# Kernel optimization log

Hardware: AMD Instinct MI355X
Metric: run time of the kernel (lower is better)

The kernel has to match this reference:

```python
import jax, jax.numpy as jnp
import numpy as np

B, L, N, M = 2, 4, 2048, 1024
K, DIV = 32, 4
S = K // DIV  # maxpool window along neighbor axis
F1 = 128      # prev features
PF = 64       # lift output point-feature dim
OUT = 256
EPS = 1e-5


def setup_inputs() -> dict:
    key = jax.random.key(0)
    ks = jax.random.split(key, 12)
    C_in = PF + F1  # 192, conv input channels
    return {
        "points": jax.random.normal(ks[0], (B, L, N, 3), jnp.float32),
        "queries": jax.random.normal(ks[1], (B, L, M, 3), jnp.float32),
        "feat_prev": jax.random.normal(ks[2], (B, L, N, F1), jnp.float32),
        # Lift params
        "bn1_g": jnp.ones((3,), jnp.float32),
        "bn1_b": jnp.zeros((3,), jnp.float32),
        "w1": jax.random.normal(ks[3], (PF // 2, 3), jnp.float32) * 0.3,
        "b1": jnp.zeros((PF // 2,), jnp.float32),
        "bn2_g": jnp.ones((PF // 2,), jnp.float32),
        "bn2_b": jnp.zeros((PF // 2,), jnp.float32),
        "w2": jax.random.normal(ks[4], (PF, PF // 2), jnp.float32) * 0.1,
        "b2": jnp.zeros((PF,), jnp.float32),
        # conv = BatchNorm3d(C_in) + Conv3d(C_in, OUT, (1,1,DIV))
        "bnc_g": jnp.ones((C_in,), jnp.float32),
        "bnc_b": jnp.zeros((C_in,), jnp.float32),
        "conv_w": jax.random.normal(ks[5], (OUT, C_in, DIV), jnp.float32) * 0.05,
        "conv_b": jnp.zeros((OUT,), jnp.float32),
    }


def _bn(x, g, b):
    """Training-mode batchnorm, channel = last axis (equivalent to the
    torch transpose(1,4)->BatchNorm3d->transpose(1,4) pattern)."""
    ax = tuple(range(x.ndim - 1))
    m = x.mean(ax)
    v = x.var(ax)  # biased variance, as torch uses for normalization
    return (x - m) * jax.lax.rsqrt(v + EPS) * g + b


_gather = jax.vmap(jax.vmap(lambda arr, idx: arr[idx]))  # over B, L


def reference(points, queries, feat_prev,
              bn1_g, bn1_b, w1, b1, bn2_g, bn2_b, w2, b2,
              bnc_g, bnc_b, conv_w, conv_b):
    # ---- KNN (cdist + topk, fully batched) ----
    pn = jnp.sum(points * points, -1)          # (B,L,N)
    qn = jnp.sum(queries * queries, -1)        # (B,L,M)
    cross = jnp.einsum('blmc,blnc->blmn', queries, points)
    d2 = qn[..., None] + pn[:, :, None, :] - 2.0 * cross  # (B,L,M,N)
    idx = jax.lax.top_k(-d2, K)[1]             # (B,L,M,K) ascending distance

    nn_pts = _gather(points, idx)              # (B,L,M,K,3)
    local = queries[:, :, :, None, :] - nn_pts # center - neighbors

    # ---- Lift MLP (with batchnorm) ----
    h = _bn(local, bn1_g, bn1_b)
    h = jax.nn.relu(jnp.einsum('blmki,oi->blmko', h, w1) + b1)
    h = _bn(h, bn2_g, bn2_b)
    h = jax.nn.relu(jnp.einsum('blmki,oi->blmko', h, w2) + b2)  # (B,L,M,K,PF)

    # ---- gather prev features, concat ----
    fp = _gather(feat_prev, idx)               # (B,L,M,K,F1)
    feat = jnp.concatenate([h, fp], axis=-1)   # (B,L,M,K,C_in)

    # ---- maxpool over neighbor shells: window S, stride S along K ----
    C = feat.shape[-1]
    fm = feat.reshape(B, L, M, DIV, S, C).max(axis=4)  # (B,L,M,DIV,C)

    # ---- BatchNorm3d(C_in) + Conv3d(C_in, OUT, (1,1,DIV)) ----
    fm = _bn(fm, bnc_g, bnc_b)
    out = jnp.einsum('blmdc,ocd->blmo', fm, conv_w) + conv_b  # (B,L,M,OUT)
    return out
```

## Files before the change

### kernel.cpp

```cpp
#include <hip/hip_runtime.h>
#include <cstdint>

#define B_    2
#define L_    4
#define N_    2048
#define M_    1024
#define K_    32
#define DIV_  4
#define S_    8
#define F1_   128
#define PF_   64
#define CIN_  192
#define OUT_  256
#define EPS_  1e-5f

#define BL_   (B_*L_)
#define BLM_  (BL_*M_)
#define NPTS_ (BLM_*K_)
#define ROWS_ (BLM_*DIV_)

#define OFF_FMH  0
#define OFF_IDX  3145728
#define OFF_LOC  3407872
#define OFF_W1F  4456448
#define OFF_B1F  4456544
#define OFF_W2F  4456576
#define OFF_B2F  4458624
#define OFF_WCB  4458688
#define OFF_BCF  4556992
#define OFF_P2   4557248
#define OFF_P3   4573632

typedef __attribute__((ext_vector_type(8))) short short8;
typedef __attribute__((ext_vector_type(4))) short short4v;
typedef __attribute__((ext_vector_type(4))) float f32x4;

__device__ __forceinline__ unsigned short f2bf(float f)
{
    unsigned u = __float_as_uint(f);
    unsigned r = (u + 0x7FFFu + ((u >> 16) & 1u)) >> 16;
    return (unsigned short)r;
}
__device__ __forceinline__ float bf2f(unsigned short h)
{
    unsigned u = ((unsigned)h) << 16;
    return __uint_as_float(u);
}

__global__ __launch_bounds__(512) void k_knn(const float* __restrict__ points,
                                             const float* __restrict__ queries,
                                             int*   __restrict__ idxbuf,
                                             float* __restrict__ local4,
                                             float* __restrict__ p1)
{
#pragma clang fp contract(off)
    __shared__ float4 pt[N_];
    __shared__ unsigned bufN[8][64];
    __shared__ float  wred[8][8];

    const int t    = threadIdx.x;
    const int lane = t & 63;
    const int wv   = t >> 6;
    const int bl   = blockIdx.x >> 7;
    const int m    = ((blockIdx.x & 127) << 3) + wv;

    const float* P = points  + (size_t)bl * (N_*3);
    const float* Q = queries + (size_t)bl * (M_*3);

    for (int n = t; n < N_; n += 512) {
        float x = P[n*3], y = P[n*3+1], z = P[n*3+2];
        float pn = (x*x + y*y) + z*z;
        pt[n] = make_float4(x, y, z, pn);
    }
    __syncthreads();

    const float qx = Q[m*3], qy = Q[m*3+1], qz = Q[m*3+2];
    const float qn = (qx*qx + qy*qy) + qz*qz;
    const double qxd = (double)qx, qyd = (double)qy, qzd = (double)qz;

    auto uAkey = [&](unsigned n) -> unsigned {
        const float4 p4 = pt[n & 2047];
        float cross = (qx*p4.x + qy*p4.y) + qz*p4.z;
        float d2f = (qn + p4.w) - 2.0f*cross;
        unsigned uA = __float_as_uint(d2f);
        return (uA & 0x80000000u) ? ~uA : (uA | 0x80000000u);
    };
    auto uBkey = [&](unsigned n) -> unsigned long long {
        const float4 p4 = pt[n & 2047];
        double dx = qxd - (double)p4.x, dy = qyd - (double)p4.y, dz = qzd - (double)p4.z;
        double d2d = dx*dx + dy*dy + dz*dz;
        unsigned long long uB = (unsigned long long)__double_as_longlong(d2d);
        uB = (uB & 0x8000000000000000ULL) ? ~uB : (uB | 0x8000000000000000ULL);
        return (uB & ~2047ULL) | (unsigned long long)(n & 2047);
    };
    auto cmp_less = [&](unsigned pa, unsigned pn, unsigned ca, unsigned cn) -> bool {
        bool eq = (pa == ca);
        bool pl = eq ? (pn < cn) : (pa < ca);
        bool realtie = eq && (ca != 0xFFFFFFFFu);
        if (realtie) pl = (uBkey(pn) < uBkey(cn));
        return pl;
    };

    unsigned Aa = 0xFFFFFFFFu;
    unsigned An = 2048u + lane;
    unsigned thrA = 0xFFFFFFFFu;
    int bufcnt = 0;

    auto flushfn = [&]() {
        unsigned sa, sn;
        if (lane < bufcnt) { sn = bufN[wv][lane]; sa = uAkey(sn); }
        else               { sa = 0xFFFFFFFFu;    sn = 2048u + lane; }
        for (int k = 2; k <= 64; k <<= 1) {
            for (int j = k >> 1; j >= 1; j >>= 1) {
                unsigned pa = __shfl_xor(sa, j);
                unsigned pn = __shfl_xor(sn, j);
                bool wantMin = (((lane & k) == 0) == ((lane & j) == 0));
                bool pl = cmp_less(pa, pn, sa, sn);
                if (pl == wantMin) { sa = pa; sn = pn; }
            }
        }
        int src = (31 - lane) & 63;
        unsigned ba = __shfl(sa, src);
        unsigned bn = __shfl(sn, src);
        if (lane < 32) {
            if (cmp_less(ba, bn, Aa, An)) { Aa = ba; An = bn; }
        }
        for (int j = 16; j >= 1; j >>= 1) {
            unsigned pa = __shfl_xor(Aa, j);
            unsigned pn = __shfl_xor(An, j);
            bool wantMin = ((lane & j) == 0);
            bool pl = cmp_less(pa, pn, Aa, An);
            if (pl == wantMin) { Aa = pa; An = pn; }
        }
        bufcnt = 0;
        thrA = __shfl(Aa, 31);
    };

    float4 p4 = pt[lane];
    for (int r = 0; r < 32; ++r) {
        const int n = r*64 + lane;
        float4 p4n = p4;
        if (r < 31) p4n = pt[n + 64];
        float cross = (qx*p4.x + qy*p4.y) + qz*p4.z;
        float d2f = (qn + p4.w) - 2.0f*cross;
        unsigned uA = __float_as_uint(d2f);
        uA = (uA & 0x80000000u) ? ~uA : (uA | 0x80000000u);
        p4 = p4n;

        bool lt = (uA <= thrA);
        unsigned long long mask = __ballot(lt);
        int cnt = __builtin_popcountll(mask);
        if (cnt == 0) continue;
        if (bufcnt + cnt > 64) {
            flushfn();
            lt = (uA <= thrA);
            mask = __ballot(lt);
            cnt = __builtin_popcountll(mask);
            if (cnt == 0) continue;
        }
        int pos = bufcnt + __builtin_popcountll(mask & ((1ULL << lane) - 1ULL));
        if (lt) bufN[wv][pos] = (unsigned)n;
        bufcnt += cnt;
    }
    if (bufcnt > 0) flushfn();

    const long long base = ((long long)bl * M_ + m) * K_;
    float lx = 0.f, ly = 0.f, lz = 0.f;
    if (lane < 32) {
        const int n = (int)An;
        idxbuf[base + lane] = n;
        const float4 pp = pt[n];
        lx = qx - pp.x; ly = qy - pp.y; lz = qz - pp.z;
        *(float4*)(local4 + (base + lane)*4) = make_float4(lx, ly, lz, 0.f);
    }
    float s0 = lx, s1 = ly, s2 = lz, s3 = lx*lx, s4 = ly*ly, s5 = lz*lz;
#pragma unroll
    for (int off = 32; off; off >>= 1) {
        s0 += __shfl_xor(s0, off); s1 += __shfl_xor(s1, off); s2 += __shfl_xor(s2, off);
        s3 += __shfl_xor(s3, off); s4 += __shfl_xor(s4, off); s5 += __shfl_xor(s5, off);
    }
    if (lane == 0) {
        wred[wv][0]=s0; wred[wv][1]=s1; wred[wv][2]=s2;
        wred[wv][3]=s3; wred[wv][4]=s4; wred[wv][5]=s5;
    }
    __syncthreads();
    if (t < 6) {
        float s = 0.f;
#pragma unroll
        for (int w = 0; w < 8; ++w) s += wred[w][t];
        p1[(long long)blockIdx.x*8 + t] = s;
    }
}

__global__ __launch_bounds__(256) void k_fold1(const float* __restrict__ p1,
                        const float* __restrict__ w1, const float* __restrict__ b1,
                        const float* __restrict__ g,  const float* __restrict__ bb,
                        float* __restrict__ w1f, float* __restrict__ b1f)
{
    __shared__ float red[6][33];
    __shared__ float s1[3], t1[3];
    const int t = threadIdx.x;
    const int c = t >> 5, i = t & 31;
    if (c < 6) {
        float s = 0.f;
        for (int w = i; w < 1024; w += 32) s += p1[w*8 + c];
        red[c][i] = s;
    }
    __syncthreads();
    if (t < 3) {
        float S = 0.f, Q = 0.f;
        for (int k = 0; k < 32; ++k) { S += red[t][k]; Q += red[t+3][k]; }
        float mean = S / (float)NPTS_;
        float var  = Q / (float)NPTS_ - mean*mean;
        float r = 1.0f / sqrtf(var + EPS_);
        float sc = r * g[t];
        s1[t] = sc; t1[t] = bb[t] - mean*sc;
    }
    __syncthreads();
    if (t < 32) {
        float acc = b1[t];
        for (int i2 = 0; i2 < 3; ++i2) {
            float w = w1[t*3+i2];
            w1f[t*3+i2] = w * s1[i2];
            acc += w * t1[i2];
        }
        b1f[t] = acc;
    }
}

__global__ __launch_bounds__(256) void k_stats2(const float* __restrict__ local4,
                                                const float* __restrict__ w1f,
                                                const float* __restrict__ b1f,
                                                float* __restrict__ p2)
{
    __shared__ float4 pts[1024];
    __shared__ float  sred[4][64];
    const int t = threadIdx.x;
    const int lane = t & 63;
    const int wv   = t >> 6;
    const int base = blockIdx.x * 1024;

    for (int j = t; j < 1024; j += 256)
        pts[j] = *(const float4*)(local4 + (size_t)(base + j) * 4);

    const int ch = lane & 31;
    const float w0 = w1f[ch*3], w1v = w1f[ch*3+1], w2v = w1f[ch*3+2];
    const float bv = b1f[ch];
    __syncthreads();

    float s = 0.f, q = 0.f;
    const int pbase = wv*256 + (lane >> 5);
    for (int it = 0; it < 128; ++it) {
        float4 v = pts[pbase + it*2];
        float h = fmaxf(bv + w0*v.x + w1v*v.y + w2v*v.z, 0.f);
        s += h; q += h*h;
    }
    s += __shfl_xor(s, 32); q += __shfl_xor(q, 32);
    if (lane < 32) { sred[wv][lane] = s; sred[wv][32+lane] = q; }
    __syncthreads();
    if (t < 64)
        p2[blockIdx.x*64 + t] = sred[0][t]+sred[1][t]+sred[2][t]+sred[3][t];
}

__global__ void k_fold2(const float* __restrict__ p2,
                        const float* __restrict__ w2, const float* __restrict__ b2,
                        const float* __restrict__ g,  const float* __restrict__ bb,
                        float* __restrict__ w2f, float* __restrict__ b2f)
{
    __shared__ float s2[32], t2[32];
    int t = threadIdx.x;
    if (t < 32) {
        float S = 0, Q = 0;
        for (int b = 0; b < 256; ++b) { S += p2[b*64+t]; Q += p2[b*64+32+t]; }
        float mean = S / (float)NPTS_;
        float var  = Q / (float)NPTS_ - mean*mean;
        float r = 1.0f / sqrtf(var + EPS_);
        float sc = r * g[t];
        s2[t] = sc; t2[t] = bb[t] - mean*sc;
    }
    __syncthreads();
    float acc = b2[t];
    for (int i = 0; i < 32; ++i) {
        float w = w2[t*32+i];
        w2f[t*32+i] = w * s2[i];
        acc += w * t2[i];
    }
    b2f[t] = acc;
}

__global__ __launch_bounds__(256) void k_shell(const float* __restrict__ feat_prev,
                                               const int*   __restrict__ idxbuf,
                                               const float* __restrict__ local4,
                                               const float* __restrict__ w1f,
                                               const float* __restrict__ b1f,
                                               const float* __restrict__ w2f,
                                               const float* __restrict__ b2f,
                                               unsigned short* __restrict__ fmh)
{
    __shared__ float w1s[96], b1s[32], b2s[64];
    __shared__ float w2s[64][33];
    __shared__ int   idxs[K_];
    __shared__ float locs[K_][4];
    __shared__ __align__(16) float h1s[K_][36];
    __shared__ float fmrow[DIV_][CIN_];

    const int t = threadIdx.x;
    const int lane = t & 63;
    const int wv   = t >> 6;

    for (int j = t; j < 2048; j += 256) { int o = j >> 5, i = j & 31; w2s[o][i] = w2f[j]; }
    if (t < 96) w1s[t] = w1f[t];
    if (t >= 96 && t < 128) b1s[t-96] = b1f[t-96];
    if (t >= 128 && t < 192) b2s[t-128] = b2f[t-128];
    __syncthreads();

    float w2c[32];
#pragma unroll
    for (int i = 0; i < 32; ++i) w2c[i] = w2s[lane][i];
    const float b2v = b2s[lane];

    for (int q = 0; q < 8; ++q) {
        const int blm = (blockIdx.x << 3) + q;
        const long long base = (long long)blm * K_;
        if (t < 32)  idxs[t] = idxbuf[base + t];
        if (t >= 64 && t < 192) ((float*)locs)[t-64] = local4[base*4 + (t-64)];
        __syncthreads();

        for (int j = t; j < 1024; j += 256) {
            int k = j >> 5, o = j & 31;
            float v = b1s[o] + w1s[o*3]*locs[k][0] + w1s[o*3+1]*locs[k][1] + w1s[o*3+2]*locs[k][2];
            h1s[k][o] = fmaxf(v, 0.f);
        }
        __syncthreads();

        {
            float mx = 0.0f;
#pragma unroll
            for (int kk = 0; kk < 8; ++kk) {
                const int k = wv*8 + kk;
                const float4* hp = (const float4*)&h1s[k][0];
                float acc = b2v;
#pragma unroll
                for (int c = 0; c < 8; ++c) {
                    float4 h4 = hp[c];
                    acc += h4.x*w2c[c*4+0];
                    acc += h4.y*w2c[c*4+1];
                    acc += h4.z*w2c[c*4+2];
                    acc += h4.w*w2c[c*4+3];
                }
                mx = fmaxf(mx, fmaxf(acc, 0.f));
            }
            fmrow[wv][lane] = mx;
        }
        {
            const float* fp0 = feat_prev + (size_t)(blm / M_) * N_ * F1_;
#pragma unroll
            for (int ph = 0; ph < 2; ++ph) {
                int d = ph*2 + (t >> 7), c = t & 127;
                float mx = -3.4e38f;
#pragma unroll
                for (int j = 0; j < 8; ++j) {
                    int n = idxs[d*8+j];
                    mx = fmaxf(mx, fp0[(size_t)n*F1_ + c]);
                }
                fmrow[d][64 + c] = mx;
            }
        }
        __syncthreads();
        for (int j = t; j < DIV_*CIN_; j += 256)
            fmh[(size_t)blm*(DIV_*CIN_) + j] = f2bf((&fmrow[0][0])[j]);
        __syncthreads();
    }
}

__global__ void k_stats3(const unsigned short* __restrict__ fmh, float* __restrict__ p3)
{
    const int t = threadIdx.x;
    const int blk = blockIdx.x;
    float s = 0.f, q = 0.f;
    const size_t base = (size_t)blk * 128 * CIN_;
    for (int r = 0; r < 128; ++r) {
        float v = bf2f(fmh[base + (size_t)r*CIN_ + t]);
        s += v; q += v*v;
    }
    p3[blk*384 + t] = s;
    p3[blk*384 + 192 + t] = q;
}

__global__ __launch_bounds__(256) void k_fold3(const float* __restrict__ p3,
                                               const float* __restrict__ conv_w,
                                               const float* __restrict__ conv_b,
                                               const float* __restrict__ g,
                                               const float* __restrict__ bb,
                                               unsigned short* __restrict__ wcfb,
                                               float* __restrict__ bcf)
{
    __shared__ float sc[CIN_], tc[CIN_];
    const int t = threadIdx.x;
    if (t < CIN_) {
        float S = 0, Q = 0;
        for (int b = 0; b < 256; ++b) { S += p3[b*384+t]; Q += p3[b*384+192+t]; }
        float mean = S / (float)ROWS_;
        float var  = Q / (float)ROWS_ - mean*mean;
        float r = 1.0f / sqrtf(var + EPS_);
        float s = r * g[t];
        sc[t] = s; tc[t] = bb[t] - mean*s;
    }
    __syncthreads();
    const int lo = blockIdx.x * 3072;
    for (int j = lo + t; j < lo + 3072; j += 256) {
        int o = j / 768, k = j - o*768;
        int d = k / CIN_, c = k - d*CIN_;
        wcfb[j] = f2bf(conv_w[o*768 + c*4 + d] * sc[c]);
    }
    if (blockIdx.x == 0) {
        float acc = conv_b[t];
        for (int c = 0; c < CIN_; ++c) {
            float tcv = tc[c];
#pragma unroll
            for (int d = 0; d < 4; ++d) acc += tcv * conv_w[t*768 + c*4 + d];
        }
        bcf[t] = acc;
    }
}

__global__ __launch_bounds__(256) void k_gemm(const unsigned short* __restrict__ A,
                                              const unsigned short* __restrict__ Wb,
                                              const float* __restrict__ bias,
                                              float* __restrict__ C)
{
    __shared__ __align__(16) unsigned short As[128][72];
    __shared__ __align__(16) unsigned short Bs[64][72];
    const int t = threadIdx.x;
    const int lane = t & 63;
    const int wv = t >> 6;
    const int row0 = (blockIdx.x >> 2) * 128;
    const int col0 = (blockIdx.x & 3) * 64;
    const int wr = wv >> 1, wc = wv & 1;
    const int r16 = lane & 15, kq = lane >> 4;

    f32x4 acc[4][2];
#pragma unroll
    for (int i = 0; i < 4; ++i)
#pragma unroll
        for (int j = 0; j < 2; ++j) acc[i][j] = (f32x4){0.f,0.f,0.f,0.f};

    for (int kt = 0; kt < 12; ++kt) {
#pragma unroll
        for (int p = 0; p < 4; ++p) {
            int j = p*256 + t;
            int r = j >> 3, kc = (j & 7) * 8;
            *(short8*)&As[r][kc] = *(const short8*)(A + (size_t)(row0 + r)*768 + kt*64 + kc);
        }
#pragma unroll
        for (int p = 0; p < 2; ++p) {
            int j = p*256 + t;
            int r = j >> 3, kc = (j & 7) * 8;
            *(short8*)&Bs[r][kc] = *(const short8*)(Wb + (size_t)(col0 + r)*768 + kt*64 + kc);
        }
        __syncthreads();
#pragma unroll
        for (int ks = 0; ks < 2; ++ks) {
            short8 bf[2];
#pragma unroll
            for (int n = 0; n < 2; ++n) {
                const unsigned short* pb = &Bs[wc*32 + n*16 + r16][ks*32 + kq*4];
                short4v b0 = *(const short4v*)pb;
                short4v b1 = *(const short4v*)(pb + 16);
                bf[n][0]=b0[0]; bf[n][1]=b0[1]; bf[n][2]=b0[2]; bf[n][3]=b0[3];
                bf[n][4]=b1[0]; bf[n][5]=b1[1]; bf[n][6]=b1[2]; bf[n][7]=b1[3];
            }
#pragma unroll
            for (int mf = 0; mf < 4; ++mf) {
                const unsigned short* pa = &As[wr*64 + mf*16 + r16][ks*32 + kq*4];
                short4v a0 = *(const short4v*)pa;
                short4v a1 = *(const short4v*)(pa + 16);
                short8 af;
                af[0]=a0[0]; af[1]=a0[1]; af[2]=a0[2]; af[3]=a0[3];
                af[4]=a1[0]; af[5]=a1[1]; af[6]=a1[2]; af[7]=a1[3];
                acc[mf][0] = __builtin_amdgcn_mfma_f32_16x16x32_bf16(af, bf[0], acc[mf][0], 0, 0, 0);
                acc[mf][1] = __builtin_amdgcn_mfma_f32_16x16x32_bf16(af, bf[1], acc[mf][1], 0, 0, 0);
            }
        }
        __syncthreads();
    }

#pragma unroll
    for (int mf = 0; mf < 4; ++mf) {
#pragma unroll
        for (int n = 0; n < 2; ++n) {
            const int col = col0 + wc*32 + n*16 + r16;
            const float bv = bias[col];
#pragma unroll
            for (int i = 0; i < 4; ++i) {
                int row = row0 + wr*64 + mf*16 + kq*4 + i;
                C[(size_t)row*256 + col] = acc[mf][n][i] + bv;
            }
        }
    }
}

extern "C" void kernel_launch(void* const* d_in, const int* in_sizes, int n_in,
                              void* d_out, int out_size, void* d_ws, size_t ws_size,
                              hipStream_t stream)
{
    const float* points    = (const float*)d_in[0];
    const float* queries   = (const float*)d_in[1];
    const float* feat_prev = (const float*)d_in[2];
    const float* bn1g = (const float*)d_in[3];
    const float* bn1b = (const float*)d_in[4];
    const float* w1   = (const float*)d_in[5];
    const float* b1   = (const float*)d_in[6];
    const float* bn2g = (const float*)d_in[7];
    const float* bn2b = (const float*)d_in[8];
    const float* w2   = (const float*)d_in[9];
    const float* b2   = (const float*)d_in[10];
    const float* bncg = (const float*)d_in[11];
    const float* bncb = (const float*)d_in[12];
    const float* convw= (const float*)d_in[13];
    const float* convb= (const float*)d_in[14];

    float* ws   = (float*)d_ws;
    unsigned short* fmh = (unsigned short*)(ws + OFF_FMH);
    int*   idxb = (int*)(ws + OFF_IDX);
    float* loc4 = ws + OFF_LOC;
    float* w1f  = ws + OFF_W1F;
    float* b1f  = ws + OFF_B1F;
    float* w2f  = ws + OFF_W2F;
    float* b2f  = ws + OFF_B2F;
    unsigned short* wcfb = (unsigned short*)(ws + OFF_WCB);
    float* bcf  = ws + OFF_BCF;
    float* p1   = ws + OFF_FMH;
    float* p2   = ws + OFF_P2;
    float* p3   = ws + OFF_P3;

    k_knn   <<<1024, 512, 0, stream>>>(points, queries, idxb, loc4, p1);
    k_fold1 <<<1, 256, 0, stream>>>(p1, w1, b1, bn1g, bn1b, w1f, b1f);
    k_stats2<<<256, 256, 0, stream>>>(loc4, w1f, b1f, p2);
    k_fold2 <<<1, 64, 0, stream>>>(p2, w2, b2, bn2g, bn2b, w2f, b2f);
    k_shell <<<BLM_/8, 256, 0, stream>>>(feat_prev, idxb, loc4, w1f, b1f, w2f, b2f, fmh);
    k_stats3<<<256, 192, 0, stream>>>(fmh, p3);
    k_fold3 <<<64, 256, 0, stream>>>(p3, convw, convb, bncg, bncb, wcfb, bcf);
    k_gemm  <<<256, 256, 0, stream>>>(fmh, wcfb, bcf, (float*)d_out);
}
```

Baseline: 173.6 us.

## Fuse BN1 fold into stats2 and BN3 statistics into shell kernel

Merges the single-block k_fold1 into k_stats2, so every block redundantly reduces the p1 partials and folds BN1 itself, with block 0 writing w1f/b1f. It also computes the per-channel sum and sum-of-squares of the bf16 pooled features inside k_shell as they are written, removing the separate k_stats3 pass that re-read fmh. This drops two launches and one full read of the pooled tensor. In exchange, k_fold3 must now reduce 1024 partial rows instead of 256 with a single thread per channel, and k_stats2 adds a redundant p1 reduction in every block.

Measured after the change: 206.2 us. 1.19x slower.

```diff
diff --git a/kernel.cpp b/kernel.cpp
--- a/kernel.cpp
+++ b/kernel.cpp
@@ -192,20 +192,35 @@
     }
 }
 
-__global__ __launch_bounds__(256) void k_fold1(const float* __restrict__ p1,
-                        const float* __restrict__ w1, const float* __restrict__ b1,
-                        const float* __restrict__ g,  const float* __restrict__ bb,
-                        float* __restrict__ w1f, float* __restrict__ b1f)
+__global__ __launch_bounds__(256) void k_stats2(const float* __restrict__ local4,
+                                                const float* __restrict__ p1,
+                                                const float* __restrict__ w1,
+                                                const float* __restrict__ b1,
+                                                const float* __restrict__ g1,
+                                                const float* __restrict__ bb1,
+                                                float* __restrict__ w1f,
+                                                float* __restrict__ b1f,
+                                                float* __restrict__ p2)
 {
     __shared__ float red[6][33];
-    __shared__ float s1[3], t1[3];
+    __shared__ float s1v[3], t1v[3];
+    __shared__ float4 pts[1024];
+    __shared__ float  sred[4][64];
     const int t = threadIdx.x;
-    const int c = t >> 5, i = t & 31;
-    if (c < 6) {
-        float s = 0.f;
-        for (int w = i; w < 1024; w += 32) s += p1[w*8 + c];
-        red[c][i] = s;
-    }
+    const int lane = t & 63;
+    const int wv   = t >> 6;
+    const int base = blockIdx.x * 1024;
+
+    {
+        const int c = t >> 5, i = t & 31;
+        if (c < 6) {
+            float s = 0.f;
+            for (int w = i; w < 1024; w += 32) s += p1[w*8 + c];
+            red[c][i] = s;
+        }
+    }
+    for (int j = t; j < 1024; j += 256)
+        pts[j] = *(const float4*)(local4 + (size_t)(base + j) * 4);
     __syncthreads();
     if (t < 3) {
         float S = 0.f, Q = 0.f;
@@ -213,40 +228,25 @@
         float mean = S / (float)NPTS_;
         float var  = Q / (float)NPTS_ - mean*mean;
         float r = 1.0f / sqrtf(var + EPS_);
-        float sc = r * g[t];
-        s1[t] = sc; t1[t] = bb[t] - mean*sc;
-    }
-    __syncthreads();
-    if (t < 32) {
+        float sc = r * g1[t];
+        s1v[t] = sc; t1v[t] = bb1[t] - mean*sc;
+    }
+    __syncthreads();
+    if (blockIdx.x == 0 && t < 32) {
         float acc = b1[t];
-        for (int i2 = 0; i2 < 3; ++i2) {
-            float w = w1[t*3+i2];
-            w1f[t*3+i2] = w * s1[i2];
-            acc += w * t1[i2];
+        for (int i = 0; i < 3; ++i) {
+            float w = w1[t*3+i];
+            w1f[t*3+i] = w * s1v[i];
+            acc += w * t1v[i];
         }
         b1f[t] = acc;
     }
-}
-
-__global__ __launch_bounds__(256) void k_stats2(const float* __restrict__ local4,
-                                                const float* __restrict__ w1f,
-                                                const float* __restrict__ b1f,
-                                                float* __restrict__ p2)
-{
-    __shared__ float4 pts[1024];
-    __shared__ float  sred[4][64];
-    const int t = threadIdx.x;
-    const int lane = t & 63;
-    const int wv   = t >> 6;
-    const int base = blockIdx.x * 1024;
-
-    for (int j = t; j < 1024; j += 256)
-        pts[j] = *(const float4*)(local4 + (size_t)(base + j) * 4);
 
     const int ch = lane & 31;
-    const float w0 = w1f[ch*3], w1v = w1f[ch*3+1], w2v = w1f[ch*3+2];
-    const float bv = b1f[ch];
-    __syncthreads();
+    const float wa = w1[ch*3], wb = w1[ch*3+1], wc = w1[ch*3+2];
+    const float w0 = wa*s1v[0], w1v = wb*s1v[1], w2v = wc*s1v[2];
+    float bv = b1[ch];
+    bv += wa*t1v[0]; bv += wb*t1v[1]; bv += wc*t1v[2];
 
     float s = 0.f, q = 0.f;
     const int pbase = wv*256 + (lane >> 5);
@@ -295,7 +295,8 @@
                                                const float* __restrict__ b1f,
                                                const float* __restrict__ w2f,
                                                const float* __restrict__ b2f,
-                                               unsigned short* __restrict__ fmh)
+                                               unsigned short* __restrict__ fmh,
+                                               float* __restrict__ p3)
 {
     __shared__ float w1s[96], b1s[32], b2s[64];
     __shared__ float w2s[64][33];
@@ -303,6 +304,7 @@
     __shared__ float locs[K_][4];
     __shared__ __align__(16) float h1s[K_][36];
     __shared__ float fmrow[DIV_][CIN_];
+    __shared__ float ps[768], pq[768];
 
     const int t = threadIdx.x;
     const int lane = t & 63;
@@ -318,6 +320,9 @@
 #pragma unroll
     for (int i = 0; i < 32; ++i) w2c[i] = w2s[lane][i];
     const float b2v = b2s[lane];
+
+    float sacc0 = 0.f, sacc1 = 0.f, sacc2 = 0.f;
+    float qacc0 = 0.f, qacc1 = 0.f, qacc2 = 0.f;
 
     for (int q = 0; q < 8; ++q) {
         const int blm = (blockIdx.x << 3) + q;
@@ -367,24 +372,31 @@
             }
         }
         __syncthreads();
-        for (int j = t; j < DIV_*CIN_; j += 256)
-            fmh[(size_t)blm*(DIV_*CIN_) + j] = f2bf((&fmrow[0][0])[j]);
+        {
+            const size_t ob = (size_t)blm*(DIV_*CIN_);
+            unsigned short h0 = f2bf((&fmrow[0][0])[t]);
+            unsigned short h1 = f2bf((&fmrow[0][0])[t+256]);
+            unsigned short h2 = f2bf((&fmrow[0][0])[t+512]);
+            fmh[ob + t]       = h0;
+            fmh[ob + t + 256] = h1;
+            fmh[ob + t + 512] = h2;
+            float v0 = bf2f(h0), v1 = bf2f(h1), v2 = bf2f(h2);
+            sacc0 += v0; qacc0 += v0*v0;
+            sacc1 += v1; qacc1 += v1*v1;
+            sacc2 += v2; qacc2 += v2*v2;
+        }
         __syncthreads();
     }
-}
-
-__global__ void k_stats3(const unsigned short* __restrict__ fmh, float* __restrict__ p3)
-{
-    const int t = threadIdx.x;
-    const int blk = blockIdx.x;
-    float s = 0.f, q = 0.f;
-    const size_t base = (size_t)blk * 128 * CIN_;
-    for (int r = 0; r < 128; ++r) {
-        float v = bf2f(fmh[base + (size_t)r*CIN_ + t]);
-        s += v; q += v*v;
-    }
-    p3[blk*384 + t] = s;
-    p3[blk*384 + 192 + t] = q;
+
+    ps[t] = sacc0; ps[t+256] = sacc1; ps[t+512] = sacc2;
+    pq[t] = qacc0; pq[t+256] = qacc1; pq[t+512] = qacc2;
+    __syncthreads();
+    if (t < CIN_) {
+        float s = ps[t] + ps[t+192] + ps[t+384] + ps[t+576];
+        float q = pq[t] + pq[t+192] + pq[t+384] + pq[t+576];
+        p3[(size_t)blockIdx.x*384 + t] = s;
+        p3[(size_t)blockIdx.x*384 + 192 + t] = q;
+    }
 }
 
 __global__ __launch_bounds__(256) void k_fold3(const float* __restrict__ p3,
@@ -399,7 +411,7 @@
     const int t = threadIdx.x;
     if (t < CIN_) {
         float S = 0, Q = 0;
-        for (int b = 0; b < 256; ++b) { S += p3[b*384+t]; Q += p3[b*384+192+t]; }
+        for (int b = 0; b < 1024; ++b) { S += p3[b*384+t]; Q += p3[b*384+192+t]; }
         float mean = S / (float)ROWS_;
         float var  = Q / (float)ROWS_ - mean*mean;
         float r = 1.0f / sqrtf(var + EPS_);
@@ -535,11 +547,9 @@
     float* p3   = ws + OFF_P3;
 
     k_knn   <<<1024, 512, 0, stream>>>(points, queries, idxb, loc4, p1);
-    k_fold1 <<<1, 256, 0, stream>>>(p1, w1, b1, bn1g, bn1b, w1f, b1f);
-    k_stats2<<<256, 256, 0, stream>>>(loc4, w1f, b1f, p2);
+    k_stats2<<<256, 256, 0, stream>>>(loc4, p1, w1, b1, bn1g, bn1b, w1f, b1f, p2);
     k_fold2 <<<1, 64, 0, stream>>>(p2, w2, b2, bn2g, bn2b, w2f, b2f);
-    k_shell <<<BLM_/8, 256, 0, stream>>>(feat_prev, idxb, loc4, w1f, b1f, w2f, b2f, fmh);
-    k_stats3<<<256, 192, 0, stream>>>(fmh, p3);
+    k_shell <<<BLM_/8, 256, 0, stream>>>(feat_prev, idxb, loc4, w1f, b1f, w2f, b2f, fmh, p3);
     k_fold3 <<<64, 256, 0, stream>>>(p3, convw, convb, bncg, bncb, wcfb, bcf);
     k_gemm  <<<256, 256, 0, stream>>>(fmh, wcfb, bcf, (float*)d_out);
 }
```
